# Performance work log

Measured on AMD Instinct MI355X. Metric: run time of the kernel, lower is better.

## Reference

```python
import jax, jax.numpy as jnp
import numpy as np

NUM_SPECIAL = 3  # rows 1..NUM_SPECIAL in special table; row 0 is padding (zeros)

def setup_inputs() -> dict:
    key = jax.random.key(0)
    ks = jax.random.split(key, 16)
    T, B, E, H, L, V = 128, 32, 512, 512, 2, 32000
    G = 4 * H
    s = 0.02
    special_emb = jax.random.normal(ks[1], (NUM_SPECIAL + 1, E), jnp.float32) * s
    special_emb = special_emb.at[0].set(0.0)  # padding_idx=0
    return {
        "ids": jax.random.randint(ks[0], (T, B), 0, V),
        "length_countdown": jax.random.uniform(ks[2], (T, B, 1), jnp.float32),
        "word_emb": jax.random.normal(ks[3], (V, E), jnp.float32) * s,
        "special_emb": special_emb,
        "h0": jax.random.normal(ks[4], (L, B, H), jnp.float32) * s,
        "c0": jax.random.normal(ks[5], (L, B, H), jnp.float32) * s,
        "prev_output": jnp.zeros((B, H), jnp.float32),
        "Wih0": jax.random.normal(ks[6], (G, E + H + 1), jnp.float32) * s,
        "Whh0": jax.random.normal(ks[7], (G, H), jnp.float32) * s,
        "bih0": jnp.zeros((G,), jnp.float32),
        "bhh0": jnp.zeros((G,), jnp.float32),
        "Wih1": jax.random.normal(ks[8], (G, H), jnp.float32) * s,
        "Whh1": jax.random.normal(ks[9], (G, H), jnp.float32) * s,
        "bih1": jnp.zeros((G,), jnp.float32),
        "bhh1": jnp.zeros((G,), jnp.float32),
        "Wg": jax.random.normal(ks[10], (V, H), jnp.float32) * s,
        "bg": jnp.zeros((V,), jnp.float32),
    }

def _lstm_cell(x, h, c, Wih, Whh, bih, bhh):
    gates = x @ Wih.T + bih + h @ Whh.T + bhh  # [B, 4H]
    i, f, g, o = jnp.split(gates, 4, axis=-1)  # torch LSTMCell gate order
    c_new = jax.nn.sigmoid(f) * c + jax.nn.sigmoid(i) * jnp.tanh(g)
    h_new = jax.nn.sigmoid(o) * jnp.tanh(c_new)
    return h_new, c_new

def reference(ids, length_countdown, word_emb, special_emb, h0, c0, prev_output,
              Wih0, Whh0, bih0, bhh0, Wih1, Whh1, bih1, bhh1, Wg, bg):
    # embeddings = word_embeddings(ids) + special_embeddings(special_ids(ids))
    sp_ids = jnp.where(ids < NUM_SPECIAL, ids + 1, 0)
    emb = word_emb[ids] + special_emb[sp_ids]                 # [T,B,E]
    rnn_in = jnp.concatenate([emb, length_countdown], axis=2)  # [T,B,E+1]

    Wihs = (Wih0, Wih1); Whhs = (Whh0, Whh1)
    bihs = (bih0, bih1); bhhs = (bhh0, bhh1)
    L = h0.shape[0]

    def step(carry, emb_t):
        out, h, c = carry
        x = jnp.concatenate([emb_t, out], axis=1)  # input feeding
        hs, cs = [], []
        for l in range(L):
            h_l, c_l = _lstm_cell(x, h[l], c[l], Wihs[l], Whhs[l], bihs[l], bhhs[l])
            x = h_l  # dropout=0
            hs.append(h_l); cs.append(c_l)
        out = x
        score = jax.nn.log_softmax(out @ Wg.T + bg, axis=-1)  # generator
        return (out, jnp.stack(hs), jnp.stack(cs)), score

    (out, hT, cT), scores = jax.lax.scan(step, (prev_output, h0, c0), rnn_in)
    return scores, (hT, cT), out
```

## Files before the change

kernel.cpp:

```cpp
#include <hip/hip_runtime.h>
#include <hip/hip_bf16.h>


typedef __attribute__((ext_vector_type(8))) short bf16x8;
typedef __attribute__((ext_vector_type(4))) float f32x4;
typedef __attribute__((ext_vector_type(2))) unsigned long long u64x2;

#define AS1 __attribute__((address_space(1)))
#define AS3 __attribute__((address_space(3)))

__device__ __forceinline__ unsigned short f2bf(float f) {
  unsigned int u = __builtin_bit_cast(unsigned int, f);
  u += 0x7fffu + ((u >> 16) & 1u);
  return (unsigned short)(u >> 16);
}

__device__ __forceinline__ void gl16(const void* g, void* l) {
  __builtin_amdgcn_global_load_lds((const AS1 unsigned int*)g,
                                   (AS3 unsigned int*)l, 16, 0, 0);
}

__device__ __forceinline__ float sigm(float x) { return 1.0f / (1.0f + __expf(-x)); }

__global__ __launch_bounds__(256, 1) void prep_k(
    const float* __restrict__ Wg,  const float* __restrict__ Wih0,
    const float* __restrict__ Whh0,const float* __restrict__ Wih1,
    const float* __restrict__ Whh1,const float* __restrict__ bih0,
    const float* __restrict__ bhh0,const float* __restrict__ bih1,
    const float* __restrict__ bhh1,const float* __restrict__ h0,
    const float* __restrict__ pout,
    unsigned short* __restrict__ WgBf, unsigned short* __restrict__ W0e,
    unsigned short* __restrict__ Wr0p, unsigned short* __restrict__ Wr1p,
    float* __restrict__ b1p, float* __restrict__ bias0c,
    float* __restrict__ wcd, unsigned short* __restrict__ A0p,
    unsigned short* __restrict__ Fp, unsigned short* __restrict__ H1p)
{
  const long N0 = 16384000L;
  const long N1 = N0 + 1048576L;
  const long N2 = N1 + 2097152L;
  const long N3 = N2 + 2097152L;
  const long N4 = N3 + 2048L;
  const long N5 = N4 + 2048L;
  const long N6 = N5 + 2048L;
  const long N7 = N6 + 49152L;
  for (long i = blockIdx.x * 256L + threadIdx.x; i < N7; i += 256L * gridDim.x) {
    if (i < N0) {
      WgBf[i] = f2bf(Wg[i]);
    } else if (i < N1) {
      long k = i - N0; int g = (int)(k >> 9); int kk = (int)(k & 511);
      W0e[k] = f2bf(Wih0[g * 1025 + kk]);
    } else if (i < N2) {
      long k = i - N1; int gp = (int)(k >> 10); int kk = (int)(k & 1023);
      int j = gp >> 2, gate = gp & 3; int g = gate * 512 + j;
      float v = (kk < 512) ? Whh0[g * 512 + kk] : Wih0[g * 1025 + 513 + (kk - 512)];
      Wr0p[k] = f2bf(v);
    } else if (i < N3) {
      long k = i - N2; int gp = (int)(k >> 10); int kk = (int)(k & 1023);
      int j = gp >> 2, gate = gp & 3; int g = gate * 512 + j;
      float v = (kk < 512) ? Wih1[g * 512 + kk] : Whh1[g * 512 + (kk - 512)];
      Wr1p[k] = f2bf(v);
    } else if (i < N4) {
      int gp = (int)(i - N3); int j = gp >> 2, gate = gp & 3; int g = gate * 512 + j;
      b1p[gp] = bih1[g] + bhh1[g];
    } else if (i < N5) {
      int g = (int)(i - N4); bias0c[g] = bih0[g] + bhh0[g];
    } else if (i < N6) {
      int g = (int)(i - N5); wcd[g] = Wih0[g * 1025 + 512];
    } else {
      long k = i - N6;
      int sub = (int)(k >> 14);
      int e = (int)(k & 16383);
      int b = e >> 9, j = e & 511;
      int off = 16384 + (j >> 3) * 256 + b * 8 + (j & 7);
      float v = (sub == 0) ? h0[b * 512 + j]
              : (sub == 1) ? pout[b * 512 + j]
                           : h0[16384 + b * 512 + j];
      unsigned short* dst = (sub == 0) ? A0p : (sub == 1) ? Fp : H1p;
      dst[off] = f2bf(v);
    }
  }
}

__global__ __launch_bounds__(256, 1) void emb_k(
    const int* __restrict__ ids, const float* __restrict__ wemb,
    const float* __restrict__ semb, unsigned short* __restrict__ ebf)
{
  const int tb = blockIdx.x;
  const int id = ids[tb];
  const int sp = (id < 3) ? (id + 1) : 0;
  const float* wr = wemb + (long)id * 512;
  const float* sr = semb + sp * 512;
  for (int i = threadIdx.x; i < 512; i += 256)
    ebf[tb * 512 + i] = f2bf(wr[i] + sr[i]);
}

template<int EPI>
__global__ __launch_bounds__(256, 1) void gemm_bt(
    const unsigned short* __restrict__ A,
    const unsigned short* __restrict__ B, int N,
    float* __restrict__ C,
    const float* __restrict__ e0, const float* __restrict__ e1,
    const float* __restrict__ e2)
{
  __shared__ unsigned short sA[4096];
  __shared__ unsigned short sB[4096];
  const int tid = threadIdx.x;
  const int l = tid & 63, w = tid >> 6;
  const int nb = N >> 7;
  const int bid = blockIdx.x;
  const int bm = bid / nb, bn = bid - bm * nb;

  const int u0 = w * 128 + l;
  const int u1 = u0 + 64;
  const int r0 = u0 >> 2, c0 = (u0 & 3) ^ (r0 & 3);
  const int r1 = u1 >> 2, c1 = (u1 & 3) ^ (r1 & 3);
  const unsigned short* ga0 = A + (long)(bm * 128 + r0) * 512 + c0 * 8;
  const unsigned short* ga1 = A + (long)(bm * 128 + r1) * 512 + c1 * 8;
  const unsigned short* gb0 = B + (long)(bn * 128 + r0) * 512 + c0 * 8;
  const unsigned short* gb1 = B + (long)(bn * 128 + r1) * 512 + c1 * 8;
  unsigned short* la0 = sA + (w * 2 + 0) * 512;
  unsigned short* la1 = sA + (w * 2 + 1) * 512;
  unsigned short* lb0 = sB + (w * 2 + 0) * 512;
  unsigned short* lb1 = sB + (w * 2 + 1) * 512;

  const int fr = l & 15, fc = l >> 4;
  const int wm = w >> 1, wn = w & 1;
  int aoff[4], boff[4];
#pragma unroll
  for (int mi = 0; mi < 4; ++mi) {
    int row = wm * 64 + mi * 16 + fr;
    aoff[mi] = row * 64 + ((fc ^ (row & 3)) * 16);
  }
#pragma unroll
  for (int ni = 0; ni < 4; ++ni) {
    int row = wn * 64 + ni * 16 + fr;
    boff[ni] = row * 64 + ((fc ^ (row & 3)) * 16);
  }

  f32x4 acc[4][4];
#pragma unroll
  for (int i = 0; i < 4; ++i)
#pragma unroll
    for (int jq = 0; jq < 4; ++jq) acc[i][jq] = (f32x4){0.f, 0.f, 0.f, 0.f};

  for (int kt = 0; kt < 16; ++kt) {
    __syncthreads();
    gl16(ga0 + kt * 32, la0);
    gl16(ga1 + kt * 32, la1);
    gl16(gb0 + kt * 32, lb0);
    gl16(gb1 + kt * 32, lb1);
    asm volatile("s_waitcnt vmcnt(0)" ::: "memory");
    __syncthreads();
    bf16x8 av[4], bv[4];
#pragma unroll
    for (int mi = 0; mi < 4; ++mi)
      av[mi] = *(const bf16x8*)((const char*)sA + aoff[mi]);
#pragma unroll
    for (int ni = 0; ni < 4; ++ni)
      bv[ni] = *(const bf16x8*)((const char*)sB + boff[ni]);
#pragma unroll
    for (int mi = 0; mi < 4; ++mi)
#pragma unroll
      for (int ni = 0; ni < 4; ++ni)
        acc[mi][ni] = __builtin_amdgcn_mfma_f32_16x16x32_bf16(av[mi], bv[ni], acc[mi][ni], 0, 0, 0);
  }

  const int mbase = bm * 128 + wm * 64;
  const int nbase = bn * 128 + wn * 64;
#pragma unroll
  for (int mi = 0; mi < 4; ++mi)
#pragma unroll
    for (int ni = 0; ni < 4; ++ni) {
      const int col = nbase + ni * 16 + fr;
#pragma unroll
      for (int r = 0; r < 4; ++r) {
        const int row = mbase + mi * 16 + fc * 4 + r;
        float v = acc[mi][ni][r];
        if (EPI == 0) {
          const int gp = ((row & 511) << 2) | (row >> 9);
          v += e0[row] + e2[col] * e1[row];
          C[(long)gp * N + col] = v;
        } else {
          v += e0[col];
          C[(long)row * N + col] = v;
        }
      }
    }
}

__global__ __launch_bounds__(256, 1) void lstm_seq(
    const unsigned short* __restrict__ Wr0p,
    const unsigned short* __restrict__ Wr1p,
    const float* __restrict__ P0t, const float* __restrict__ b1p,
    const float* __restrict__ h0in, const float* __restrict__ c0in,
    unsigned short* __restrict__ A0p, unsigned short* __restrict__ Fp,
    unsigned short* __restrict__ H1p,
    unsigned short* __restrict__ outbf, float* __restrict__ outs,
    unsigned int* __restrict__ flagA, unsigned int* __restrict__ flagB)
{
  const int tid = threadIdx.x;
  const int wg = blockIdx.x;
  const int l = tid & 63, w = tid >> 6;
  const int mi = w & 1, ni = w >> 1;
  const int fr = l & 15, fc = l >> 4;

  __shared__ unsigned short sx[32768];
  __shared__ float sg[32][33];
  __shared__ unsigned short sh[32][8];

  const int b = tid & 31, jl = tid >> 5;
  const int j = wg * 8 + jl;

  float c0r = c0in[b * 512 + j];
  float c1r = c0in[16384 + b * 512 + j];
  float h0keep = 0.0f, h1keep = 0.0f;

  float b1v0 = b1p[j * 4 + 0], b1v1 = b1p[j * 4 + 1];
  float b1v2 = b1p[j * 4 + 2], b1v3 = b1p[j * 4 + 3];

  const int xrow = mi * 16 + fr;
  const char* sxb = (const char*)sx + xrow * 2048;
  const int xr = (xrow & 7) << 4;
  const int brow = (wg * 32 + ni * 16 + fr) * 1024 + fc * 8;

  const int srow = tid & 31;
  const int swz = (srow & 7) << 4;
  char* const sxw = (char*)sx + srow * 2048;
  const int wgj0 = tid >> 5;

#define STAGE(srcp, half)                                                     \
  do {                                                                        \
    unsigned long long q0[8], q1[8];                                          \
    _Pragma("unroll")                                                         \
    for (int i = 0; i < 8; ++i) {                                             \
      int u = i * 256 + tid;                                                  \
      q0[i] = __hip_atomic_load((const unsigned long long*)(srcp) + u * 2,    \
                                __ATOMIC_RELAXED, __HIP_MEMORY_SCOPE_AGENT);  \
      q1[i] = __hip_atomic_load((const unsigned long long*)(srcp) + u * 2 + 1,\
                                __ATOMIC_RELAXED, __HIP_MEMORY_SCOPE_AGENT);  \
    }                                                                         \
    _Pragma("unroll")                                                         \
    for (int i = 0; i < 8; ++i) {                                             \
      int cb = (half) * 1024 + (i * 8 + wgj0) * 16;                           \
      u64x2 v; v.x = q0[i]; v.y = q1[i];                                      \
      *(u64x2*)(sxw + (cb ^ swz)) = v;                                        \
    }                                                                         \
  } while (0)

#define MFMA_HALF(Wp, k0, accv)                                               \
  do {                                                                        \
    _Pragma("unroll")                                                         \
    for (int kt = (k0); kt < (k0) + 16; ++kt) {                               \
      bf16x8 av = *(const bf16x8*)(sxb + ((kt * 64 + fc * 16) ^ xr));         \
      bf16x8 bv = *(const bf16x8*)((Wp) + brow + kt * 32);                    \
      accv = __builtin_amdgcn_mfma_f32_16x16x32_bf16(av, bv, accv, 0, 0, 0);  \
    }                                                                         \
  } while (0)

  for (int t = 0; t < 128; ++t) {
    const int pw = t & 1;
    const int pr = (t + 1) & 1;

    float p0a = P0t[(j * 4 + 0) * 4096 + t * 32 + b];
    float p0b = P0t[(j * 4 + 1) * 4096 + t * 32 + b];
    float p0c = P0t[(j * 4 + 2) * 4096 + t * 32 + b];
    float p0d = P0t[(j * 4 + 3) * 4096 + t * 32 + b];

    f32x4 accA = (f32x4){0.f, 0.f, 0.f, 0.f};
    STAGE(A0p + pr * 16384, 0);
    __syncthreads();
    MFMA_HALF(Wr0p, 0, accA);

    {
      for (;;) {
        unsigned int f = __hip_atomic_load(&flagB[l << 5], __ATOMIC_RELAXED, __HIP_MEMORY_SCOPE_AGENT);
        if (__all((int)(f >= (unsigned int)t))) break;
        __builtin_amdgcn_s_sleep(1);
      }
      asm volatile("" ::: "memory");
    }
    STAGE(Fp + pr * 16384, 1);
    __syncthreads();
    MFMA_HALF(Wr0p, 16, accA);
#pragma unroll
    for (int r = 0; r < 4; ++r) sg[mi * 16 + fc * 4 + r][ni * 16 + fr] = accA[r];
    __syncthreads();
    {
      float gi = sg[b][jl * 4 + 0] + p0a;
      float gf = sg[b][jl * 4 + 1] + p0b;
      float gg = sg[b][jl * 4 + 2] + p0c;
      float go = sg[b][jl * 4 + 3] + p0d;
      float cn = sigm(gf) * c0r + sigm(gi) * tanhf(gg);
      float hn = sigm(go) * tanhf(cn);
      c0r = cn; h0keep = hn;
      sh[b][jl] = f2bf(hn);
    }
    __syncthreads();
    if (w == 0) {
      if (l < 32) {
        u64x2 v = *(const u64x2*)&sh[l][0];
        unsigned long long* dst = (unsigned long long*)(A0p + pw * 16384 + wg * 256 + l * 8);
        __hip_atomic_store(dst,     v.x, __ATOMIC_RELAXED, __HIP_MEMORY_SCOPE_AGENT);
        __hip_atomic_store(dst + 1, v.y, __ATOMIC_RELAXED, __HIP_MEMORY_SCOPE_AGENT);
      }
      asm volatile("s_waitcnt vmcnt(0)" ::: "memory");
      if (tid == 0)
        __hip_atomic_store(&flagA[wg << 5], (unsigned int)(t + 1), __ATOMIC_RELAXED, __HIP_MEMORY_SCOPE_AGENT);
    }

    f32x4 accB = (f32x4){0.f, 0.f, 0.f, 0.f};
    STAGE(H1p + pr * 16384, 1);
    __syncthreads();
    MFMA_HALF(Wr1p, 16, accB);

    {
      for (;;) {
        unsigned int f = __hip_atomic_load(&flagA[l << 5], __ATOMIC_RELAXED, __HIP_MEMORY_SCOPE_AGENT);
        if (__all((int)(f >= (unsigned int)(t + 1)))) break;
        __builtin_amdgcn_s_sleep(1);
      }
      asm volatile("" ::: "memory");
    }
    STAGE(A0p + pw * 16384, 0);
    __syncthreads();
    MFMA_HALF(Wr1p, 0, accB);
#pragma unroll
    for (int r = 0; r < 4; ++r) sg[mi * 16 + fc * 4 + r][ni * 16 + fr] = accB[r];
    __syncthreads();
    {
      float gi = sg[b][jl * 4 + 0] + b1v0;
      float gf = sg[b][jl * 4 + 1] + b1v1;
      float gg = sg[b][jl * 4 + 2] + b1v2;
      float go = sg[b][jl * 4 + 3] + b1v3;
      float cn = sigm(gf) * c1r + sigm(gi) * tanhf(gg);
      float hn = sigm(go) * tanhf(cn);
      c1r = cn; h1keep = hn;
      sh[b][jl] = f2bf(hn);
      outbf[(t * 32 + b) * 512 + j] = f2bf(hn);
    }
    __syncthreads();
    if (w == 0) {
      const int bb = l & 31;
      unsigned short* base = (l < 32) ? (Fp + pw * 16384) : (H1p + pw * 16384);
      u64x2 v = *(const u64x2*)&sh[bb][0];
      unsigned long long* dst = (unsigned long long*)(base + wg * 256 + bb * 8);
      __hip_atomic_store(dst,     v.x, __ATOMIC_RELAXED, __HIP_MEMORY_SCOPE_AGENT);
      __hip_atomic_store(dst + 1, v.y, __ATOMIC_RELAXED, __HIP_MEMORY_SCOPE_AGENT);
      asm volatile("s_waitcnt vmcnt(0)" ::: "memory");
      if (tid == 0)
        __hip_atomic_store(&flagB[wg << 5], (unsigned int)(t + 1), __ATOMIC_RELAXED, __HIP_MEMORY_SCOPE_AGENT);
    }
  }
#undef STAGE
#undef MFMA_HALF

  float* hT = outs + 131072000;
  float* cT = outs + 131072000 + 32768;
  float* oT = outs + 131072000 + 65536;
  hT[b * 512 + j] = h0keep;
  hT[16384 + b * 512 + j] = h1keep;
  cT[b * 512 + j] = c0r;
  cT[16384 + b * 512 + j] = c1r;
  oT[b * 512 + j] = h1keep;
}

__global__ __launch_bounds__(256, 1) void lse_fix(float* __restrict__ sc)
{
  const long row = blockIdx.x;
  float4* p4 = (float4*)(sc + row * 32000L);
  const int tid = threadIdx.x;
  float m = -3.0e38f, s = 0.0f;
  for (int i = tid; i < 8000; i += 256) {
    float4 v = p4[i];
    float m4 = fmaxf(fmaxf(v.x, v.y), fmaxf(v.z, v.w));
    float mn = fmaxf(m, m4);
    s = s * __expf(m - mn) + __expf(v.x - mn) + __expf(v.y - mn)
        + __expf(v.z - mn) + __expf(v.w - mn);
    m = mn;
  }
#pragma unroll
  for (int off = 32; off > 0; off >>= 1) {
    float mo = __shfl_down(m, off);
    float so = __shfl_down(s, off);
    float mn = fmaxf(m, mo);
    s = s * __expf(m - mn) + so * __expf(mo - mn);
    m = mn;
  }
  __shared__ float lm[4], ls[4], lse_sh;
  if ((tid & 63) == 0) { lm[tid >> 6] = m; ls[tid >> 6] = s; }
  __syncthreads();
  if (tid == 0) {
    float M = lm[0], S = ls[0];
#pragma unroll
    for (int i = 1; i < 4; ++i) {
      float mn = fmaxf(M, lm[i]);
      S = S * __expf(M - mn) + ls[i] * __expf(lm[i] - mn);
      M = mn;
    }
    lse_sh = M + __logf(S);
  }
  __syncthreads();
  const float lse = lse_sh;
  for (int i = tid; i < 8000; i += 256) {
    float4 v = p4[i];
    v.x -= lse; v.y -= lse; v.z -= lse; v.w -= lse;
    p4[i] = v;
  }
}

extern "C" void kernel_launch(void* const* d_in, const int* in_sizes, int n_in,
                              void* d_out, int out_size, void* d_ws, size_t ws_size,
                              hipStream_t stream) {
  const int*   ids  = (const int*)d_in[0];
  const float* cd   = (const float*)d_in[1];
  const float* wemb = (const float*)d_in[2];
  const float* semb = (const float*)d_in[3];
  const float* h0   = (const float*)d_in[4];
  const float* c0   = (const float*)d_in[5];
  const float* pout = (const float*)d_in[6];
  const float* Wih0 = (const float*)d_in[7];
  const float* Whh0 = (const float*)d_in[8];
  const float* bih0 = (const float*)d_in[9];
  const float* bhh0 = (const float*)d_in[10];
  const float* Wih1 = (const float*)d_in[11];
  const float* Whh1 = (const float*)d_in[12];
  const float* bih1 = (const float*)d_in[13];
  const float* bhh1 = (const float*)d_in[14];
  const float* Wg   = (const float*)d_in[15];
  const float* bg   = (const float*)d_in[16];
  float* out = (float*)d_out;

  char* ws = (char*)d_ws;
  unsigned short* WgBf   = (unsigned short*)(ws);
  unsigned short* W0e    = (unsigned short*)(ws + 32768000);
  unsigned short* Wr0p   = (unsigned short*)(ws + 34865152);
  unsigned short* Wr1p   = (unsigned short*)(ws + 39059456);
  float*          b1p    = (float*)(ws + 43253760);
  float*          bias0c = (float*)(ws + 43261952);
  float*          wcd    = (float*)(ws + 43270144);
  unsigned short* embbf  = (unsigned short*)(ws + 43409408);
  unsigned short* outbf  = (unsigned short*)(ws + 47603712);
  float*          P0t    = (float*)(ws + 51798016);
  unsigned int*   flagA  = (unsigned int*)(ws + 85352448);
  unsigned int*   flagB  = (unsigned int*)(ws + 85360640);
  unsigned short* A0p    = (unsigned short*)(ws + 85368832);
  unsigned short* Fp     = (unsigned short*)(ws + 85434368);
  unsigned short* H1p    = (unsigned short*)(ws + 85499904);

  hipMemsetAsync((void*)flagA, 0, 16384, stream);

  prep_k<<<8192, 256, 0, stream>>>(Wg, Wih0, Whh0, Wih1, Whh1,
                                   bih0, bhh0, bih1, bhh1, h0, pout,
                                   WgBf, W0e, Wr0p, Wr1p, b1p, bias0c, wcd,
                                   A0p, Fp, H1p);

  emb_k<<<4096, 256, 0, stream>>>(ids, wemb, semb, embbf);

  gemm_bt<0><<<512, 256, 0, stream>>>(W0e, embbf, 4096, P0t, bias0c, wcd, cd);

  lstm_seq<<<64, 256, 0, stream>>>(Wr0p, Wr1p, P0t, b1p, h0, c0,
                                   A0p, Fp, H1p, outbf, out, flagA, flagB);

  gemm_bt<1><<<8000, 256, 0, stream>>>(outbf, WgBf, 32000, out, bg, nullptr, nullptr);

  lse_fix<<<4096, 256, 0, stream>>>(out);
}
```

Baseline: 1.997 ms.

## Halve persistent LSTM workgroups and drop double-buffered hidden-state exchange

The persistent recurrent kernel now runs on 32 workgroups instead of 64, each owning 16 hidden units. Each wave computes two 16-row MFMA tiles that share one weight fragment. Hidden states are exchanged through single-buffered global arrays laid out per workgroup, with flag values offset so readers wait for the matching step. A prologue stages the initial layer-0 state. The aim is to cut cross-workgroup synchronisation fan-in and per-step polling. The cost is twice the MFMA and weight-load work per workgroup on the serial critical path, and single buffering risks overwrite races.

Result: faster. 1.956 ms (-2.0%).

```diff
diff --git a/kernel.cpp b/kernel.cpp
--- a/kernel.cpp
+++ b/kernel.cpp
@@ -32,8 +32,8 @@
     unsigned short* __restrict__ WgBf, unsigned short* __restrict__ W0e,
     unsigned short* __restrict__ Wr0p, unsigned short* __restrict__ Wr1p,
     float* __restrict__ b1p, float* __restrict__ bias0c,
-    float* __restrict__ wcd, unsigned short* __restrict__ A0p,
-    unsigned short* __restrict__ Fp, unsigned short* __restrict__ H1p)
+    float* __restrict__ wcd, unsigned short* __restrict__ H0X,
+    unsigned short* __restrict__ FOUT, unsigned short* __restrict__ H1I)
 {
   const long N0 = 16384000L;
   const long N1 = N0 + 1048576L;
@@ -70,13 +70,13 @@
       long k = i - N6;
       int sub = (int)(k >> 14);
       int e = (int)(k & 16383);
-      int b = e >> 9, j = e & 511;
-      int off = 16384 + (j >> 3) * 256 + b * 8 + (j & 7);
+      int wgx = e >> 9, b = (e >> 4) & 31, jl = e & 15;
+      int j = wgx * 16 + jl;
       float v = (sub == 0) ? h0[b * 512 + j]
-              : (sub == 1) ? pout[b * 512 + j]
-                           : h0[16384 + b * 512 + j];
-      unsigned short* dst = (sub == 0) ? A0p : (sub == 1) ? Fp : H1p;
-      dst[off] = f2bf(v);
+              : (sub == 1) ? h0[16384 + b * 512 + j]
+                           : pout[b * 512 + j];
+      unsigned short* dst = (sub == 0) ? H0X : (sub == 1) ? H1I : FOUT;
+      dst[e] = f2bf(v);
     }
   }
 }
@@ -192,43 +192,48 @@
     const unsigned short* __restrict__ Wr0p,
     const unsigned short* __restrict__ Wr1p,
     const float* __restrict__ P0t, const float* __restrict__ b1p,
-    const float* __restrict__ h0in, const float* __restrict__ c0in,
-    unsigned short* __restrict__ A0p, unsigned short* __restrict__ Fp,
-    unsigned short* __restrict__ H1p,
+    const float* __restrict__ c0in,
+    unsigned short* __restrict__ H0X, unsigned short* __restrict__ H1X,
+    const unsigned short* __restrict__ FOUT, const unsigned short* __restrict__ H1I,
     unsigned short* __restrict__ outbf, float* __restrict__ outs,
     unsigned int* __restrict__ flagA, unsigned int* __restrict__ flagB)
 {
   const int tid = threadIdx.x;
   const int wg = blockIdx.x;
   const int l = tid & 63, w = tid >> 6;
-  const int mi = w & 1, ni = w >> 1;
   const int fr = l & 15, fc = l >> 4;
 
   __shared__ unsigned short sx[32768];
-  __shared__ float sg[32][33];
-  __shared__ unsigned short sh[32][8];
-
-  const int b = tid & 31, jl = tid >> 5;
-  const int j = wg * 8 + jl;
-
-  float c0r = c0in[b * 512 + j];
-  float c1r = c0in[16384 + b * 512 + j];
-  float h0keep = 0.0f, h1keep = 0.0f;
-
-  float b1v0 = b1p[j * 4 + 0], b1v1 = b1p[j * 4 + 1];
-  float b1v2 = b1p[j * 4 + 2], b1v3 = b1p[j * 4 + 3];
-
-  const int xrow = mi * 16 + fr;
-  const char* sxb = (const char*)sx + xrow * 2048;
-  const int xr = (xrow & 7) << 4;
-  const int brow = (wg * 32 + ni * 16 + fr) * 1024 + fc * 8;
-
-  const int srow = tid & 31;
-  const int swz = (srow & 7) << 4;
-  char* const sxw = (char*)sx + srow * 2048;
-  const int wgj0 = tid >> 5;
-
-#define STAGE(srcp, half)                                                     \
+  __shared__ float sg[32][65];
+  __shared__ unsigned short sh[32][16];
+
+  const int b = tid & 31, jl0 = tid >> 5;
+  const int sb = l >> 1, sjh = l & 1;
+
+  float c0r[2], c1r[2], h0k[2], h1k[2];
+#pragma unroll
+  for (int jq = 0; jq < 2; ++jq) {
+    c0r[jq] = c0in[b * 512 + wg * 16 + jl0 + jq * 8];
+    c1r[jq] = c0in[16384 + b * 512 + wg * 16 + jl0 + jq * 8];
+    h0k[jq] = 0.f; h1k[jq] = 0.f;
+  }
+
+  float b1v[8];
+#pragma unroll
+  for (int jq = 0; jq < 2; ++jq)
+#pragma unroll
+    for (int g = 0; g < 4; ++g)
+      b1v[jq * 4 + g] = b1p[(wg * 16 + jl0 + jq * 8) * 4 + g];
+
+  const char* sxb0 = (const char*)sx + fr * 2048;
+  const char* sxb1 = (const char*)sx + (16 + fr) * 2048;
+  const int xr = (fr & 7) << 4;
+  const int wrow = (wg * 64 + w * 16 + fr) * 1024 + fc * 8;
+
+  char* const sxw = (char*)sx + sb * 2048;
+  const int sswz = (sb & 7) << 4;
+
+#define STAGE2(srcp, half)                                                    \
   do {                                                                        \
     unsigned long long q0[8], q1[8];                                          \
     _Pragma("unroll")                                                         \
@@ -241,127 +246,151 @@
     }                                                                         \
     _Pragma("unroll")                                                         \
     for (int i = 0; i < 8; ++i) {                                             \
-      int cb = (half) * 1024 + (i * 8 + wgj0) * 16;                           \
+      int cb = (half) * 1024 + (i * 4 + w) * 32 + sjh * 16;                   \
       u64x2 v; v.x = q0[i]; v.y = q1[i];                                      \
-      *(u64x2*)(sxw + (cb ^ swz)) = v;                                        \
+      *(u64x2*)(sxw + (cb ^ sswz)) = v;                                       \
     }                                                                         \
   } while (0)
 
-#define MFMA_HALF(Wp, k0, accv)                                               \
+#define MFMA_HALF(Wp, k0, a0v, a1v)                                           \
   do {                                                                        \
     _Pragma("unroll")                                                         \
     for (int kt = (k0); kt < (k0) + 16; ++kt) {                               \
-      bf16x8 av = *(const bf16x8*)(sxb + ((kt * 64 + fc * 16) ^ xr));         \
-      bf16x8 bv = *(const bf16x8*)((Wp) + brow + kt * 32);                    \
-      accv = __builtin_amdgcn_mfma_f32_16x16x32_bf16(av, bv, accv, 0, 0, 0);  \
+      bf16x8 bv = *(const bf16x8*)((Wp) + wrow + kt * 32);                    \
+      bf16x8 x0 = *(const bf16x8*)(sxb0 + ((kt * 64 + fc * 16) ^ xr));        \
+      bf16x8 x1 = *(const bf16x8*)(sxb1 + ((kt * 64 + fc * 16) ^ xr));        \
+      a0v = __builtin_amdgcn_mfma_f32_16x16x32_bf16(x0, bv, a0v, 0, 0, 0);    \
+      a1v = __builtin_amdgcn_mfma_f32_16x16x32_bf16(x1, bv, a1v, 0, 0, 0);    \
     }                                                                         \
   } while (0)
 
+#define POLL(flags, tgt)                                                      \
+  do {                                                                        \
+    const unsigned int* fp = (flags) + ((l & 31) << 5);                       \
+    for (;;) {                                                                \
+      unsigned int f = __hip_atomic_load(fp, __ATOMIC_RELAXED,                \
+                                         __HIP_MEMORY_SCOPE_AGENT);           \
+      if (__all((int)(f >= (unsigned int)(tgt)))) break;                      \
+      __builtin_amdgcn_s_sleep(1);                                            \
+    }                                                                         \
+    asm volatile("" ::: "memory");                                            \
+  } while (0)
+
+  STAGE2(H0X, 0);
+  __syncthreads();
+  if (tid == 0)
+    __hip_atomic_store(&flagB[wg << 5], 1u, __ATOMIC_RELAXED, __HIP_MEMORY_SCOPE_AGENT);
+
   for (int t = 0; t < 128; ++t) {
-    const int pw = t & 1;
-    const int pr = (t + 1) & 1;
-
-    float p0a = P0t[(j * 4 + 0) * 4096 + t * 32 + b];
-    float p0b = P0t[(j * 4 + 1) * 4096 + t * 32 + b];
-    float p0c = P0t[(j * 4 + 2) * 4096 + t * 32 + b];
-    float p0d = P0t[(j * 4 + 3) * 4096 + t * 32 + b];
-
-    f32x4 accA = (f32x4){0.f, 0.f, 0.f, 0.f};
-    STAGE(A0p + pr * 16384, 0);
-    __syncthreads();
-    MFMA_HALF(Wr0p, 0, accA);
-
-    {
-      for (;;) {
-        unsigned int f = __hip_atomic_load(&flagB[l << 5], __ATOMIC_RELAXED, __HIP_MEMORY_SCOPE_AGENT);
-        if (__all((int)(f >= (unsigned int)t))) break;
-        __builtin_amdgcn_s_sleep(1);
-      }
-      asm volatile("" ::: "memory");
-    }
-    STAGE(Fp + pr * 16384, 1);
-    __syncthreads();
-    MFMA_HALF(Wr0p, 16, accA);
-#pragma unroll
-    for (int r = 0; r < 4; ++r) sg[mi * 16 + fc * 4 + r][ni * 16 + fr] = accA[r];
-    __syncthreads();
-    {
-      float gi = sg[b][jl * 4 + 0] + p0a;
-      float gf = sg[b][jl * 4 + 1] + p0b;
-      float gg = sg[b][jl * 4 + 2] + p0c;
-      float go = sg[b][jl * 4 + 3] + p0d;
-      float cn = sigm(gf) * c0r + sigm(gi) * tanhf(gg);
+    float p0v[8];
+#pragma unroll
+    for (int jq = 0; jq < 2; ++jq)
+#pragma unroll
+      for (int g = 0; g < 4; ++g)
+        p0v[jq * 4 + g] =
+            P0t[(long)((wg * 16 + jl0 + jq * 8) * 4 + g) * 4096 + t * 32 + b];
+
+    f32x4 accA0 = (f32x4){0.f, 0.f, 0.f, 0.f};
+    f32x4 accA1 = (f32x4){0.f, 0.f, 0.f, 0.f};
+    MFMA_HALF(Wr0p, 0, accA0, accA1);
+
+    POLL(flagB, t + 1);
+    if (t == 0) STAGE2(FOUT, 1); else STAGE2(H1X, 1);
+    __syncthreads();
+    MFMA_HALF(Wr0p, 16, accA0, accA1);
+#pragma unroll
+    for (int r = 0; r < 4; ++r) {
+      sg[fc * 4 + r][w * 16 + fr] = accA0[r];
+      sg[16 + fc * 4 + r][w * 16 + fr] = accA1[r];
+    }
+    __syncthreads();
+#pragma unroll
+    for (int jq = 0; jq < 2; ++jq) {
+      const int jl = jl0 + jq * 8;
+      float gi = sg[b][jl * 4 + 0] + p0v[jq * 4 + 0];
+      float gf = sg[b][jl * 4 + 1] + p0v[jq * 4 + 1];
+      float gg = sg[b][jl * 4 + 2] + p0v[jq * 4 + 2];
+      float go = sg[b][jl * 4 + 3] + p0v[jq * 4 + 3];
+      float cn = sigm(gf) * c0r[jq] + sigm(gi) * tanhf(gg);
       float hn = sigm(go) * tanhf(cn);
-      c0r = cn; h0keep = hn;
+      c0r[jq] = cn; h0k[jq] = hn;
       sh[b][jl] = f2bf(hn);
     }
     __syncthreads();
     if (w == 0) {
-      if (l < 32) {
-        u64x2 v = *(const u64x2*)&sh[l][0];
-        unsigned long long* dst = (unsigned long long*)(A0p + pw * 16384 + wg * 256 + l * 8);
-        __hip_atomic_store(dst,     v.x, __ATOMIC_RELAXED, __HIP_MEMORY_SCOPE_AGENT);
-        __hip_atomic_store(dst + 1, v.y, __ATOMIC_RELAXED, __HIP_MEMORY_SCOPE_AGENT);
-      }
-      asm volatile("s_waitcnt vmcnt(0)" ::: "memory");
-      if (tid == 0)
-        __hip_atomic_store(&flagA[wg << 5], (unsigned int)(t + 1), __ATOMIC_RELAXED, __HIP_MEMORY_SCOPE_AGENT);
-    }
-
-    f32x4 accB = (f32x4){0.f, 0.f, 0.f, 0.f};
-    STAGE(H1p + pr * 16384, 1);
-    __syncthreads();
-    MFMA_HALF(Wr1p, 16, accB);
-
-    {
-      for (;;) {
-        unsigned int f = __hip_atomic_load(&flagA[l << 5], __ATOMIC_RELAXED, __HIP_MEMORY_SCOPE_AGENT);
-        if (__all((int)(f >= (unsigned int)(t + 1)))) break;
-        __builtin_amdgcn_s_sleep(1);
-      }
-      asm volatile("" ::: "memory");
-    }
-    STAGE(A0p + pw * 16384, 0);
-    __syncthreads();
-    MFMA_HALF(Wr1p, 0, accB);
-#pragma unroll
-    for (int r = 0; r < 4; ++r) sg[mi * 16 + fc * 4 + r][ni * 16 + fr] = accB[r];
-    __syncthreads();
-    {
-      float gi = sg[b][jl * 4 + 0] + b1v0;
-      float gf = sg[b][jl * 4 + 1] + b1v1;
-      float gg = sg[b][jl * 4 + 2] + b1v2;
-      float go = sg[b][jl * 4 + 3] + b1v3;
-      float cn = sigm(gf) * c1r + sigm(gi) * tanhf(gg);
-      float hn = sigm(go) * tanhf(cn);
-      c1r = cn; h1keep = hn;
-      sh[b][jl] = f2bf(hn);
-      outbf[(t * 32 + b) * 512 + j] = f2bf(hn);
-    }
-    __syncthreads();
-    if (w == 0) {
-      const int bb = l & 31;
-      unsigned short* base = (l < 32) ? (Fp + pw * 16384) : (H1p + pw * 16384);
-      u64x2 v = *(const u64x2*)&sh[bb][0];
-      unsigned long long* dst = (unsigned long long*)(base + wg * 256 + bb * 8);
+      u64x2 v = *(const u64x2*)&sh[sb][sjh * 8];
+      unsigned long long* dst =
+          (unsigned long long*)(H0X + wg * 512 + sb * 16 + sjh * 8);
       __hip_atomic_store(dst,     v.x, __ATOMIC_RELAXED, __HIP_MEMORY_SCOPE_AGENT);
       __hip_atomic_store(dst + 1, v.y, __ATOMIC_RELAXED, __HIP_MEMORY_SCOPE_AGENT);
       asm volatile("s_waitcnt vmcnt(0)" ::: "memory");
       if (tid == 0)
-        __hip_atomic_store(&flagB[wg << 5], (unsigned int)(t + 1), __ATOMIC_RELAXED, __HIP_MEMORY_SCOPE_AGENT);
-    }
-  }
-#undef STAGE
+        __hip_atomic_store(&flagA[wg << 5], (unsigned int)(t + 1),
+                           __ATOMIC_RELAXED, __HIP_MEMORY_SCOPE_AGENT);
+    }
+
+    f32x4 accB0 = (f32x4){0.f, 0.f, 0.f, 0.f};
+    f32x4 accB1 = (f32x4){0.f, 0.f, 0.f, 0.f};
+    if (t == 0) {
+      STAGE2(H1I, 1);
+      __syncthreads();
+    }
+    MFMA_HALF(Wr1p, 16, accB0, accB1);
+
+    POLL(flagA, t + 1);
+    STAGE2(H0X, 0);
+    __syncthreads();
+    MFMA_HALF(Wr1p, 0, accB0, accB1);
+#pragma unroll
+    for (int r = 0; r < 4; ++r) {
+      sg[fc * 4 + r][w * 16 + fr] = accB0[r];
+      sg[16 + fc * 4 + r][w * 16 + fr] = accB1[r];
+    }
+    __syncthreads();
+#pragma unroll
+    for (int jq = 0; jq < 2; ++jq) {
+      const int jl = jl0 + jq * 8;
+      float gi = sg[b][jl * 4 + 0] + b1v[jq * 4 + 0];
+      float gf = sg[b][jl * 4 + 1] + b1v[jq * 4 + 1];
+      float gg = sg[b][jl * 4 + 2] + b1v[jq * 4 + 2];
+      float go = sg[b][jl * 4 + 3] + b1v[jq * 4 + 3];
+      float cn = sigm(gf) * c1r[jq] + sigm(gi) * tanhf(gg);
+      float hn = sigm(go) * tanhf(cn);
+      c1r[jq] = cn; h1k[jq] = hn;
+      sh[b][jl] = f2bf(hn);
+    }
+    __syncthreads();
+    if (w == 0) {
+      u64x2 v = *(const u64x2*)&sh[sb][sjh * 8];
+      unsigned long long* dst =
+          (unsigned long long*)(H1X + wg * 512 + sb * 16 + sjh * 8);
+      __hip_atomic_store(dst,     v.x, __ATOMIC_RELAXED, __HIP_MEMORY_SCOPE_AGENT);
+      __hip_atomic_store(dst + 1, v.y, __ATOMIC_RELAXED, __HIP_MEMORY_SCOPE_AGENT);
+      asm volatile("s_waitcnt vmcnt(0)" ::: "memory");
+      if (tid == 0)
+        __hip_atomic_store(&flagB[wg << 5], (unsigned int)(t + 2),
+                           __ATOMIC_RELAXED, __HIP_MEMORY_SCOPE_AGENT);
+    } else if (w == 1) {
+      u64x2 v = *(const u64x2*)&sh[sb][sjh * 8];
+      *(u64x2*)(outbf + (t * 32 + sb) * 512 + wg * 16 + sjh * 8) = v;
+    }
+  }
+#undef STAGE2
 #undef MFMA_HALF
+#undef POLL
 
   float* hT = outs + 131072000;
   float* cT = outs + 131072000 + 32768;
   float* oT = outs + 131072000 + 65536;
-  hT[b * 512 + j] = h0keep;
-  hT[16384 + b * 512 + j] = h1keep;
-  cT[b * 512 + j] = c0r;
-  cT[16384 + b * 512 + j] = c1r;
-  oT[b * 512 + j] = h1keep;
+#pragma unroll
+  for (int jq = 0; jq < 2; ++jq) {
+    const int j = wg * 16 + jl0 + jq * 8;
+    hT[b * 512 + j] = h0k[jq];
+    hT[16384 + b * 512 + j] = h1k[jq];
+    cT[b * 512 + j] = c0r[jq];
+    cT[16384 + b * 512 + j] = c1r[jq];
+    oT[b * 512 + j] = h1k[jq];
+  }
 }
 
 __global__ __launch_bounds__(256, 1) void lse_fix(float* __restrict__ sc)
@@ -442,24 +471,25 @@
   unsigned short* outbf  = (unsigned short*)(ws + 47603712);
   float*          P0t    = (float*)(ws + 51798016);
   unsigned int*   flagA  = (unsigned int*)(ws + 85352448);
-  unsigned int*   flagB  = (unsigned int*)(ws + 85360640);
-  unsigned short* A0p    = (unsigned short*)(ws + 85368832);
-  unsigned short* Fp     = (unsigned short*)(ws + 85434368);
-  unsigned short* H1p    = (unsigned short*)(ws + 85499904);
-
-  hipMemsetAsync((void*)flagA, 0, 16384, stream);
+  unsigned int*   flagB  = (unsigned int*)(ws + 85356544);
+  unsigned short* H0X    = (unsigned short*)(ws + 85360640);
+  unsigned short* H1X    = (unsigned short*)(ws + 85393408);
+  unsigned short* FOUT   = (unsigned short*)(ws + 85426176);
+  unsigned short* H1I    = (unsigned short*)(ws + 85458944);
+
+  hipMemsetAsync((void*)flagA, 0, 8192, stream);
 
   prep_k<<<8192, 256, 0, stream>>>(Wg, Wih0, Whh0, Wih1, Whh1,
                                    bih0, bhh0, bih1, bhh1, h0, pout,
                                    WgBf, W0e, Wr0p, Wr1p, b1p, bias0c, wcd,
-                                   A0p, Fp, H1p);
+                                   H0X, FOUT, H1I);
 
   emb_k<<<4096, 256, 0, stream>>>(ids, wemb, semb, embbf);
 
   gemm_bt<0><<<512, 256, 0, stream>>>(W0e, embbf, 4096, P0t, bias0c, wcd, cd);
 
-  lstm_seq<<<64, 256, 0, stream>>>(Wr0p, Wr1p, P0t, b1p, h0, c0,
-                                   A0p, Fp, H1p, outbf, out, flagA, flagB);
+  lstm_seq<<<32, 256, 0, stream>>>(Wr0p, Wr1p, P0t, b1p, c0,
+                                   H0X, H1X, FOUT, H1I, outbf, out, flagA, flagB);
 
   gemm_bt<1><<<8000, 256, 0, stream>>>(outbf, WgBf, 32000, out, bg, nullptr, nullptr);
 
```
